# Optimization experiments

Hardware: AMD Instinct MI355X
Metric: run time of the kernel (lower is better)

The kernel has to match this reference:

```python
import jax, jax.numpy as jnp
import numpy as np

T, H = 2048, 1024          # tokens, hidden_size
NH, NKV, D = 16, 4, 64     # heads, kv heads, head_dim
E, F = 8, 1024             # experts, intermediate_size
TOPK = 1
EPS = 1e-5
THETA = 500000.0
SCALE = D ** -0.5


def rmsnorm(x, w=None, eps=EPS):
    # fp32 accumulation like vLLM RMSNorm
    v = jnp.mean(x.astype(jnp.float32) ** 2, axis=-1, keepdims=True)
    y = x.astype(jnp.float32) * jax.lax.rsqrt(v + eps)
    y = y.astype(x.dtype)
    return y * w if w is not None else y


def setup_inputs() -> dict:
    key = jax.random.key(0)
    ks = jax.random.split(key, 12)
    s = 1.0 / np.sqrt(H)
    sf = 1.0 / np.sqrt(F)
    return {
        "positions": jnp.arange(T, dtype=jnp.int32),
        "hidden_states": jax.random.normal(ks[0], (T, H), jnp.float32),
        "ln1_w": jnp.ones((H,), jnp.float32),
        "ln2_w": jnp.ones((H,), jnp.float32),
        "wqkv": jax.random.normal(ks[1], (H, (NH + 2 * NKV) * D), jnp.float32) * s,
        "wo": jax.random.normal(ks[2], (NH * D, H), jnp.float32) * s,
        "router_w": jax.random.normal(ks[3], (H, E), jnp.float32) * s,
        "w_gate": jax.random.normal(ks[4], (E, H, F), jnp.float32) * s,
        "w_up": jax.random.normal(ks[5], (E, H, F), jnp.float32) * s,
        "w_down": jax.random.normal(ks[6], (E, F, H), jnp.float32) * sf,
        "sh_gate": jax.random.normal(ks[7], (H, F), jnp.float32) * s,
        "sh_up": jax.random.normal(ks[8], (H, F), jnp.float32) * s,
        "sh_down": jax.random.normal(ks[9], (F, H), jnp.float32) * sf,
    }


def reference(positions, hidden_states, ln1_w, ln2_w, wqkv, wo, router_w,
              w_gate, w_up, w_down, sh_gate, sh_up, sh_down):
    # --- input_layernorm (residual is None on first call) ---
    residual = hidden_states
    h = rmsnorm(hidden_states, ln1_w)

    # --- attention: qkv proj ---
    qkv = h @ wqkv
    q = qkv[:, : NH * D].reshape(T, NH, D)
    k = qkv[:, NH * D: (NH + NKV) * D].reshape(T, NKV, D)
    v = qkv[:, (NH + NKV) * D:].reshape(T, NKV, D)

    # --- neox-style RoPE ---
    half = D // 2
    inv_freq = 1.0 / (THETA ** (jnp.arange(half, dtype=jnp.float32) / half))
    ang = positions.astype(jnp.float32)[:, None] * inv_freq[None, :]
    cos = jnp.cos(ang)[:, None, :]  # [T,1,half]
    sin = jnp.sin(ang)[:, None, :]

    def rope(x):
        x1, x2 = x[..., :half], x[..., half:]
        return jnp.concatenate([x1 * cos - x2 * sin, x2 * cos + x1 * sin], axis=-1)

    q = rope(q)
    k = rope(k)

    # --- fp32 QK-RMSNorm (no weight), applied after RoPE as in source ---
    q = rmsnorm(q)
    k = rmsnorm(k)

    # --- GQA causal attention ---
    n_rep = NH // NKV
    kr = jnp.repeat(k, n_rep, axis=1)  # [T,NH,D]
    vr = jnp.repeat(v, n_rep, axis=1)
    scores = jnp.einsum('thd,shd->hts', q, kr) * SCALE  # [NH,T,T]
    causal = positions[:, None] >= positions[None, :]
    scores = jnp.where(causal[None], scores, -jnp.inf)
    attn = jax.nn.softmax(scores, axis=-1)
    ao = jnp.einsum('hts,shd->thd', attn, vr).reshape(T, NH * D)
    h = ao @ wo

    # --- post_attention_layernorm with fused residual add ---
    x = h + residual
    residual = x
    h = rmsnorm(x, ln2_w)

    # --- MoE: top-1 sigmoid router, router weight applied on input ---
    logits = h @ router_w                      # [T,E]
    score, idx = jax.lax.top_k(logits, TOPK)   # [T,1]
    gate = jax.nn.sigmoid(score.astype(jnp.float32)).astype(h.dtype)
    x_in = h * gate                            # apply_router_weight_on_input
    onehot = (idx == jnp.arange(E)[None, :]).astype(h.dtype)  # [T,E]
    g = jax.nn.silu(jnp.einsum('th,ehf->tef', x_in, w_gate)) \
        * jnp.einsum('th,ehf->tef', x_in, w_up)               # [T,E,F]
    out_e = jnp.einsum('tef,efh->teh', g, w_down)             # [T,E,H]
    routed = jnp.einsum('teh,te->th', out_e, onehot)

    # --- shared expert (SiLU MLP) ---
    shared = (jax.nn.silu(h @ sh_gate) * (h @ sh_up)) @ sh_down

    out = routed + shared
    return (out, residual)
```

## Files before the change

kernel.cpp:

```cpp
#include <hip/hip_runtime.h>
#include <hip/hip_bf16.h>
#include <cmath>
#include <cstdint>

#define T 2048
#define H 1024
#define NH 16
#define NKV 4
#define DH 64
#define NE 8
#define FF 1024
#define QKVN ((NH + 2 * NKV) * DH)
#define EPS 1e-5f
#define ATTN_SCALE 0.125f
#define LOG2E 1.44269504f
#define MBOUND 12.0f
#define ASPLIT 4

typedef short bf16x8 __attribute__((ext_vector_type(8)));
typedef float floatx4 __attribute__((ext_vector_type(4)));

#define VMCNT(n) asm volatile("s_waitcnt vmcnt(" #n ")" ::: "memory")

__device__ __forceinline__ void gload16(const void* g, void* l) {
  __builtin_amdgcn_global_load_lds((const __attribute__((address_space(1))) void*)g,
                                   (__attribute__((address_space(3))) void*)l, 16, 0, 0);
}

__global__ __launch_bounds__(256) void rmsnorm1024(const float* __restrict__ x,
                                                   const float* __restrict__ w,
                                                   __hip_bfloat16* __restrict__ yb) {
  int row = blockIdx.x;
  const float4* x4 = (const float4*)(x + (size_t)row * H);
  float4 v = x4[threadIdx.x];
  float s = v.x * v.x + v.y * v.y + v.z * v.z + v.w * v.w;
  #pragma unroll
  for (int o = 32; o; o >>= 1) s += __shfl_down(s, o, 64);
  __shared__ float red[4];
  if ((threadIdx.x & 63) == 0) red[threadIdx.x >> 6] = s;
  __syncthreads();
  s = red[0] + red[1] + red[2] + red[3];
  float inv = rsqrtf(s * (1.0f / (float)H) + EPS);
  float4 wv = ((const float4*)w)[threadIdx.x];
  __hip_bfloat16* yp = yb + (size_t)row * H + threadIdx.x * 4;
  yp[0] = __float2bfloat16(v.x * inv * wv.x);
  yp[1] = __float2bfloat16(v.y * inv * wv.y);
  yp[2] = __float2bfloat16(v.z * inv * wv.z);
  yp[3] = __float2bfloat16(v.w * inv * wv.w);
}

__global__ __launch_bounds__(256) void fused_add_rms(const float* __restrict__ a,
                                                     const float* __restrict__ b,
                                                     float* __restrict__ resid,
                                                     const float* __restrict__ w,
                                                     float* __restrict__ yf,
                                                     __hip_bfloat16* __restrict__ yb,
                                                     int* __restrict__ counts_g) {
  int row = blockIdx.x;
  if (row == 0 && threadIdx.x < 2 * NE) counts_g[threadIdx.x] = 0;
  float4 av = ((const float4*)(a + (size_t)row * H))[threadIdx.x];
  float4 bv = ((const float4*)(b + (size_t)row * H))[threadIdx.x];
  float4 v = make_float4(av.x + bv.x, av.y + bv.y, av.z + bv.z, av.w + bv.w);
  ((float4*)(resid + (size_t)row * H))[threadIdx.x] = v;
  float s = v.x * v.x + v.y * v.y + v.z * v.z + v.w * v.w;
  #pragma unroll
  for (int o = 32; o; o >>= 1) s += __shfl_down(s, o, 64);
  __shared__ float red[4];
  if ((threadIdx.x & 63) == 0) red[threadIdx.x >> 6] = s;
  __syncthreads();
  s = red[0] + red[1] + red[2] + red[3];
  float inv = rsqrtf(s * (1.0f / (float)H) + EPS);
  float4 wv = ((const float4*)w)[threadIdx.x];
  float o0 = v.x * inv * wv.x, o1 = v.y * inv * wv.y, o2 = v.z * inv * wv.z, o3 = v.w * inv * wv.w;
  ((float4*)(yf + (size_t)row * H))[threadIdx.x] = make_float4(o0, o1, o2, o3);
  __hip_bfloat16* yp = yb + (size_t)row * H + threadIdx.x * 4;
  yp[0] = __float2bfloat16(o0);
  yp[1] = __float2bfloat16(o1);
  yp[2] = __float2bfloat16(o2);
  yp[3] = __float2bfloat16(o3);
}

__global__ __launch_bounds__(256) void tcast9(const float* __restrict__ srcE,
                                              const float* __restrict__ srcS,
                                              __hip_bfloat16* __restrict__ dst, int R, int C,
                                              long long srcStride, long long dstStride,
                                              long long sBatch, long long dBatch) {
  int z = blockIdx.z;
  const float* src = (srcS && z == (int)gridDim.z - 1) ? srcS : srcE + (long long)z * sBatch;
  dst += (long long)z * dBatch;
  int c0 = blockIdx.x * 64, r0 = blockIdx.y * 32;
  __shared__ float tile[32][65];
  int tid = threadIdx.x;
  int lr = tid >> 4;
  int lc = (tid & 15) * 4;
  #pragma unroll
  for (int it = 0; it < 2; it++) {
    float4 v = *(const float4*)(src + (long long)(r0 + lr + it * 16) * srcStride + c0 + lc);
    tile[lr + it * 16][lc + 0] = v.x;
    tile[lr + it * 16][lc + 1] = v.y;
    tile[lr + it * 16][lc + 2] = v.z;
    tile[lr + it * 16][lc + 3] = v.w;
  }
  __syncthreads();
  int oc = tid >> 2;
  int rr = (tid & 3) * 8;
  short ov[8];
  #pragma unroll
  for (int i = 0; i < 8; i++) {
    __hip_bfloat16 b = __float2bfloat16(tile[rr + i][oc]);
    ov[i] = *(short*)&b;
  }
  *(bf16x8*)((short*)dst + (long long)(c0 + oc) * dstStride + r0 + rr) = *(bf16x8*)ov;
}

__global__ __launch_bounds__(256) void gemm_bf16(const __hip_bfloat16* __restrict__ A,
                                                 const __hip_bfloat16* __restrict__ A2,
                                                 const __hip_bfloat16* __restrict__ Bt,
                                                 void* __restrict__ Cout, void* __restrict__ Cout2,
                                                 int M, int N, int K, int out_bf16,
                                                 const int* __restrict__ row_offs,
                                                 long long strideB,
                                                 const int* __restrict__ permA,
                                                 const float* __restrict__ gatev) {
  int e = blockIdx.z;
  bool sh = (A2 != nullptr && e == (int)gridDim.z - 1);
  int rbeg = 0, rend = M;
  const __hip_bfloat16* Ap = A;
  void* Cp = Cout;
  const int* pA = permA;
  if (sh) {
    Ap = A2; Cp = Cout2; pA = nullptr;
  } else if (row_offs) {
    rbeg = row_offs[e]; rend = row_offs[e + 1];
  }
  long long m0 = rbeg + (long long)blockIdx.y * 128;
  if (m0 >= rend) return;
  long long n0 = (long long)blockIdx.x * 64;
  const __hip_bfloat16* Bp = Bt + (long long)e * strideB;

  __shared__ unsigned short As[3 * 128 * 64];
  __shared__ unsigned short Bs[3 * 64 * 64];

  int tid = threadIdx.x;
  int lane = tid & 63, w = tid >> 6;
  int wr = (w >> 1) * 64, wc = (w & 1) * 32;
  int qd = lane >> 4, ln16 = lane & 15;
  int l7 = ln16 & 7;

  floatx4 acc[4][2];
  floatx4 zero = {0.f, 0.f, 0.f, 0.f};
  #pragma unroll
  for (int i = 0; i < 4; i++)
    #pragma unroll
    for (int j = 0; j < 2; j++) acc[i][j] = zero;

  int rowA[4], kcA[4];
  const unsigned short* Arow[4];
  const unsigned short* Brow[2];
  #pragma unroll
  for (int it = 0; it < 4; it++) {
    int chunk = tid + it * 256;
    rowA[it] = chunk >> 3;
    kcA[it] = ((chunk & 7) ^ (rowA[it] & 7)) * 8;
    long long ra = m0 + rowA[it];
    if (ra >= rend) ra = rend - 1;
    long long tok = pA ? (long long)pA[ra] : ra;
    Arow[it] = (const unsigned short*)Ap + tok * K;
  }
  #pragma unroll
  for (int it = 0; it < 2; it++)
    Brow[it] = (const unsigned short*)Bp + (n0 + rowA[it]) * K;

  auto stage = [&](int j) {
    int slot = j % 3;
    int kk = j << 6;
    unsigned short* Ad = As + slot * 8192;
    unsigned short* Bd = Bs + slot * 4096;
    #pragma unroll
    for (int it = 0; it < 4; it++)
      gload16(Arow[it] + kk + kcA[it], Ad + (tid + it * 256) * 8);
    #pragma unroll
    for (int it = 0; it < 2; it++)
      gload16(Brow[it] + kk + kcA[it], Bd + (tid + it * 256) * 8);
  };

  int NT = K >> 6;
  stage(0);
  if (NT > 1) { stage(1); VMCNT(6); } else { VMCNT(0); }
  __builtin_amdgcn_s_barrier();
  __builtin_amdgcn_sched_barrier(0);

  for (int k = 0; k < NT; k++) {
    if (k + 2 < NT) stage(k + 2);
    __builtin_amdgcn_sched_barrier(0);
    const unsigned short* Ac = As + (k % 3) * 8192;
    const unsigned short* Bc = Bs + (k % 3) * 4096;
    #pragma unroll
    for (int s = 0; s < 2; s++) {
      bf16x8 af[4], bfr[2];
      #pragma unroll
      for (int i = 0; i < 4; i++) {
        int row = wr + i * 16 + ln16;
        af[i] = *(const bf16x8*)(Ac + row * 64 + (((s * 4 + qd) ^ l7) * 8));
      }
      #pragma unroll
      for (int j = 0; j < 2; j++) {
        int row = wc + j * 16 + ln16;
        bfr[j] = *(const bf16x8*)(Bc + row * 64 + (((s * 4 + qd) ^ l7) * 8));
      }
      #pragma unroll
      for (int i = 0; i < 4; i++)
        #pragma unroll
        for (int j = 0; j < 2; j++)
          acc[i][j] = __builtin_amdgcn_mfma_f32_16x16x32_bf16(af[i], bfr[j], acc[i][j], 0, 0, 0);
    }
    if (k + 1 < NT) {
      if (k + 2 < NT) { VMCNT(6); } else { VMCNT(0); }
      __builtin_amdgcn_s_barrier();
      __builtin_amdgcn_sched_barrier(0);
    }
  }

  #pragma unroll
  for (int i = 0; i < 4; i++) {
    #pragma unroll
    for (int r = 0; r < 4; r++) {
      long long gm = m0 + wr + i * 16 + qd * 4 + r;
      if (gm < rend) {
        float gsc = 1.0f;
        if (pA && gatev) gsc = gatev[pA[gm]];
        #pragma unroll
        for (int j = 0; j < 2; j++) {
          long long gn = n0 + wc + j * 16 + ln16;
          float v = acc[i][j][r] * gsc;
          if (out_bf16)
            ((__hip_bfloat16*)Cp)[gm * N + gn] = __float2bfloat16(v);
          else
            ((float*)Cp)[gm * N + gn] = v;
        }
      }
    }
  }
}

__global__ __launch_bounds__(256) void rope_pack(const float* __restrict__ qkv,
                                                 const int* __restrict__ positions,
                                                 __hip_bfloat16* __restrict__ Qb,
                                                 __hip_bfloat16* __restrict__ Kb) {
  int b = blockIdx.x * 4 + (threadIdx.x >> 6);
  int t = b / (NH + NKV);
  int hh = b % (NH + NKV);
  const float* ptr = qkv + (long long)t * QKVN + hh * DH;
  int d = threadIdx.x & 63;
  float v = ptr[d];
  int fi = d & 31;
  float inv_freq = exp2f(-(float)fi * (18.93156857f / 32.0f));
  float ang = (float)positions[t] * inv_freq;
  float c = __cosf(ang), s = __sinf(ang);
  float other = __shfl_xor(v, 32, 64);
  float r = (d < 32) ? (v * c - other * s) : (v * c + other * s);
  float sq = r * r;
  #pragma unroll
  for (int off = 32; off; off >>= 1) sq += __shfl_xor(sq, off, 64);
  float o = r * rsqrtf(sq * (1.0f / (float)DH) + EPS);
  if (hh < NH)
    Qb[(size_t)t * (NH * DH) + hh * DH + d] = __float2bfloat16(o * (ATTN_SCALE * LOG2E));
  else
    Kb[(size_t)t * (NKV * DH) + (hh - NH) * DH + d] = __float2bfloat16(o);
}

__global__ __launch_bounds__(256, 2) void attn_mfma(const __hip_bfloat16* __restrict__ Qb,
                                                    const __hip_bfloat16* __restrict__ Kbuf,
                                                    const __hip_bfloat16* __restrict__ VtG,
                                                    float* __restrict__ Opart,
                                                    float* __restrict__ Lpart) {
  int kvh = blockIdx.y;
  int qi = blockIdx.x;
  int sp = blockIdx.z;
  int q0 = qi * 64;
  int nt = qi + 1;
  if (sp >= nt) return;
  int NT = (nt - 1 - sp) / ASPLIT + 1;

  __shared__ unsigned short Ks[3 * 64 * 64];
  __shared__ unsigned short Vs[3 * 64 * 64];
  __shared__ unsigned short Ps[4 * 16 * 64];

  int tid = threadIdx.x;
  int lane = tid & 63, w = tid >> 6;
  int h = kvh * 4 + w;
  int qd = lane >> 4, ln16 = lane & 15;
  int l7 = ln16 & 7;
  unsigned short* Pw = Ps + w * 16 * 64;

  int r0 = tid >> 3;
  int sc = ((tid & 7) ^ (r0 & 7)) * 8;

  const unsigned short* KbP = (const unsigned short*)Kbuf;
  const unsigned short* VtP = (const unsigned short*)VtG;

  auto stage = [&](int k) {
    int kb = (sp + k * ASPLIT) * 64;
    int slot = k % 3;
    unsigned short* Kd = Ks + slot * 4096;
    unsigned short* Vd = Vs + slot * 4096;
    gload16(KbP + (size_t)(kb + r0) * (NKV * DH) + kvh * DH + sc, Kd + tid * 8);
    gload16(KbP + (size_t)(kb + r0 + 32) * (NKV * DH) + kvh * DH + sc, Kd + tid * 8 + 2048);
    gload16(VtP + (size_t)(kvh * DH + r0) * T + kb + sc, Vd + tid * 8);
    gload16(VtP + (size_t)(kvh * DH + r0 + 32) * T + kb + sc, Vd + tid * 8 + 2048);
  };

  bf16x8 aq[4][2];
  #pragma unroll
  for (int rt = 0; rt < 4; rt++) {
    const unsigned short* qp =
        (const unsigned short*)Qb + (size_t)(q0 + rt * 16 + ln16) * (NH * DH) + h * DH;
    aq[rt][0] = *(const bf16x8*)(qp + qd * 8);
    aq[rt][1] = *(const bf16x8*)(qp + 32 + qd * 8);
  }

  bf16x8 ones;
  #pragma unroll
  for (int i = 0; i < 8; i++) ones[i] = (short)0x3F80;

  floatx4 O_[4][4], accl[4];
  floatx4 zero = {0.f, 0.f, 0.f, 0.f};
  #pragma unroll
  for (int rt = 0; rt < 4; rt++) {
    #pragma unroll
    for (int j = 0; j < 4; j++) O_[rt][j] = zero;
    accl[rt] = zero;
  }

  stage(0);
  if (NT > 1) { stage(1); VMCNT(4); } else { VMCNT(0); }
  __builtin_amdgcn_s_barrier();
  __builtin_amdgcn_sched_barrier(0);

  for (int k = 0; k < NT; k++) {
    if (k + 2 < NT) stage(k + 2);
    __builtin_amdgcn_sched_barrier(0);
    const unsigned short* Kc = Ks + (k % 3) * 4096;
    const unsigned short* Vc = Vs + (k % 3) * 4096;
    int kb = (sp + k * ASPLIT) * 64;

    #pragma unroll
    for (int rt = 0; rt < 4; rt++) {
      floatx4 S_[4];
      #pragma unroll
      for (int j = 0; j < 4; j++) S_[j] = zero;
      #pragma unroll
      for (int s = 0; s < 2; s++) {
        bf16x8 bk[4];
        #pragma unroll
        for (int j = 0; j < 4; j++)
          bk[j] = *(const bf16x8*)(Kc + (j * 16 + ln16) * 64 + (((s * 4 + qd) ^ l7) * 8));
        #pragma unroll
        for (int j = 0; j < 4; j++)
          S_[j] = __builtin_amdgcn_mfma_f32_16x16x32_bf16(aq[rt][s], bk[j], S_[j], 0, 0, 0);
      }

      int tq_base = q0 + rt * 16 + qd * 4;
      if (kb + 63 > q0 + rt * 16) {
        #pragma unroll
        for (int j = 0; j < 4; j++) {
          int tk = kb + j * 16 + ln16;
          #pragma unroll
          for (int r = 0; r < 4; r++)
            S_[j][r] = (tk <= tq_base + r) ? exp2f(S_[j][r] - MBOUND) : 0.f;
        }
      } else {
        #pragma unroll
        for (int j = 0; j < 4; j++)
          #pragma unroll
          for (int r = 0; r < 4; r++) S_[j][r] = exp2f(S_[j][r] - MBOUND);
      }

      #pragma unroll
      for (int j = 0; j < 4; j++)
        #pragma unroll
        for (int r = 0; r < 4; r++) {
          int row = qd * 4 + r;
          int pc = (((j * 2 + (ln16 >> 3)) ^ (row & 7)) * 8) + l7;
          __hip_bfloat16 pb = __float2bfloat16(S_[j][r]);
          Pw[row * 64 + pc] = *(unsigned short*)&pb;
        }

      #pragma unroll
      for (int s = 0; s < 2; s++) {
        bf16x8 ap = *(const bf16x8*)(Pw + ln16 * 64 + (((s * 4 + qd) ^ l7) * 8));
        bf16x8 bv[4];
        #pragma unroll
        for (int j = 0; j < 4; j++)
          bv[j] = *(const bf16x8*)(Vc + (j * 16 + ln16) * 64 + (((s * 4 + qd) ^ l7) * 8));
        #pragma unroll
        for (int j = 0; j < 4; j++)
          O_[rt][j] = __builtin_amdgcn_mfma_f32_16x16x32_bf16(ap, bv[j], O_[rt][j], 0, 0, 0);
        accl[rt] = __builtin_amdgcn_mfma_f32_16x16x32_bf16(ap, ones, accl[rt], 0, 0, 0);
      }
    }
    if (k + 1 < NT) {
      if (k + 2 < NT) { VMCNT(4); } else { VMCNT(0); }
      __builtin_amdgcn_s_barrier();
      __builtin_amdgcn_sched_barrier(0);
    }
  }

  size_t pbase = ((size_t)(qi * NH + h) * ASPLIT + sp) * (64 * 64);
  #pragma unroll
  for (int rt = 0; rt < 4; rt++) {
    int rl_base = rt * 16 + qd * 4;
    #pragma unroll
    for (int j = 0; j < 4; j++)
      #pragma unroll
      for (int r = 0; r < 4; r++)
        Opart[pbase + (size_t)(rl_base + r) * 64 + j * 16 + ln16] = O_[rt][j][r];
  }
  if (ln16 == 0) {
    size_t lbase = ((size_t)(qi * NH + h) * ASPLIT + sp) * 64;
    #pragma unroll
    for (int rt = 0; rt < 4; rt++)
      #pragma unroll
      for (int r = 0; r < 4; r++) Lpart[lbase + rt * 16 + qd * 4 + r] = accl[rt][r];
  }
}

__global__ __launch_bounds__(256) void attn_combine(const float* __restrict__ Opart,
                                                    const float* __restrict__ Lpart,
                                                    __hip_bfloat16* __restrict__ ao) {
  int qi = blockIdx.x, h = blockIdx.y;
  int nv = (qi + 1 < ASPLIT) ? (qi + 1) : ASPLIT;
  int row = threadIdx.x >> 2;
  int c0 = (threadIdx.x & 3) * 16;
  size_t base = (size_t)(qi * NH + h) * ASPLIT * 4096;
  size_t lb = (size_t)(qi * NH + h) * ASPLIT * 64;
  float l = 0.f;
  float acc[16];
  #pragma unroll
  for (int i = 0; i < 16; i++) acc[i] = 0.f;
  for (int s = 0; s < nv; s++) {
    const float* Op = Opart + base + (size_t)s * 4096 + (size_t)row * 64 + c0;
    l += Lpart[lb + s * 64 + row];
    #pragma unroll
    for (int i = 0; i < 16; i += 4) {
      float4 v = *(const float4*)(Op + i);
      acc[i] += v.x; acc[i + 1] += v.y; acc[i + 2] += v.z; acc[i + 3] += v.w;
    }
  }
  float inv = 1.f / l;
  int t = qi * 64 + row;
  short ov[16];
  #pragma unroll
  for (int i = 0; i < 16; i++) {
    __hip_bfloat16 b = __float2bfloat16(acc[i] * inv);
    ov[i] = *(short*)&b;
  }
  short* dst = (short*)ao + (size_t)t * (NH * DH) + h * DH + c0;
  *(bf16x8*)dst = *(bf16x8*)&ov[0];
  *(bf16x8*)(dst + 8) = *(bf16x8*)&ov[8];
}

__global__ void silumul_both(const __hip_bfloat16* __restrict__ gA2,
                             const __hip_bfloat16* __restrict__ gS2,
                             __hip_bfloat16* __restrict__ gP,
                             __hip_bfloat16* __restrict__ gPs, int n4each) {
  int i = blockIdx.x * blockDim.x + threadIdx.x;
  const __hip_bfloat16* src = gA2;
  __hip_bfloat16* dst = gP;
  if (i >= n4each) {
    i -= n4each;
    src = gS2;
    dst = gPs;
  }
  int el = i * 4;
  int row = el >> 10;
  int c = el & (FF - 1);
  const __hip_bfloat16* g = src + (size_t)row * (2 * FF) + c;
  #pragma unroll
  for (int k = 0; k < 4; k++) {
    float av = __bfloat162float(g[k]);
    float bv = __bfloat162float(g[FF + k]);
    dst[el + k] = __float2bfloat16(av / (1.f + __expf(-av)) * bv);
  }
}

__global__ __launch_bounds__(64) void router_kernel(const float* __restrict__ h2,
                                                    const float* __restrict__ rw,
                                                    int* __restrict__ idx,
                                                    float* __restrict__ gate,
                                                    int* __restrict__ counts) {
  int t = blockIdx.x;
  int lane = threadIdx.x;
  float acc[NE] = {};
  for (int k = lane; k < H; k += 64) {
    float hv = h2[(long long)t * H + k];
    float4 r0 = *(const float4*)(rw + (long long)k * NE);
    float4 r1 = *(const float4*)(rw + (long long)k * NE + 4);
    acc[0] += hv * r0.x; acc[1] += hv * r0.y; acc[2] += hv * r0.z; acc[3] += hv * r0.w;
    acc[4] += hv * r1.x; acc[5] += hv * r1.y; acc[6] += hv * r1.z; acc[7] += hv * r1.w;
  }
  #pragma unroll
  for (int off = 32; off; off >>= 1)
    #pragma unroll
    for (int e2 = 0; e2 < NE; e2++) acc[e2] += __shfl_down(acc[e2], off, 64);
  if (lane == 0) {
    int best = 0;
    float bv = acc[0];
    #pragma unroll
    for (int e2 = 1; e2 < NE; e2++)
      if (acc[e2] > bv) { bv = acc[e2]; best = e2; }
    idx[t] = best;
    gate[t] = 1.f / (1.f + expf(-bv));
    atomicAdd(&counts[best], 1);
  }
}

__global__ __launch_bounds__(256) void assign_scan(const int* __restrict__ counts,
                                                   const int* __restrict__ idx,
                                                   int* __restrict__ offs,
                                                   int* __restrict__ cnt2,
                                                   int* __restrict__ perm,
                                                   int* __restrict__ pos) {
  __shared__ int offs_s[NE + 1];
  if (threadIdx.x == 0) {
    int s = 0;
    for (int e2 = 0; e2 < NE; e2++) { offs_s[e2] = s; offs[e2] = s; s += counts[e2]; }
    offs_s[NE] = s; offs[NE] = s;
  }
  __syncthreads();
  for (int t = threadIdx.x; t < T; t += 256) {
    int e2 = idx[t];
    int p = offs_s[e2] + atomicAdd(&cnt2[e2], 1);
    pos[t] = p;
    perm[p] = t;
  }
}

__global__ __launch_bounds__(256) void final_add_kernel(float* __restrict__ out,
                                                        const float* __restrict__ outp,
                                                        const int* __restrict__ pos) {
  int t = blockIdx.x;
  int p = pos[t];
  const float4* src = (const float4*)(outp + (long long)p * H);
  float4* dst = (float4*)(out + (long long)t * H);
  float4 a = dst[threadIdx.x];
  float4 b = src[threadIdx.x];
  a.x += b.x; a.y += b.y; a.z += b.z; a.w += b.w;
  dst[threadIdx.x] = a;
}

extern "C" void kernel_launch(void* const* d_in, const int* in_sizes, int n_in,
                              void* d_out, int out_size, void* d_ws, size_t ws_size,
                              hipStream_t stream) {
  const int* positions = (const int*)d_in[0];
  const float* hidden = (const float*)d_in[1];
  const float* ln1_w = (const float*)d_in[2];
  const float* ln2_w = (const float*)d_in[3];
  const float* wqkv = (const float*)d_in[4];
  const float* wo = (const float*)d_in[5];
  const float* router_w = (const float*)d_in[6];
  const float* w_gate = (const float*)d_in[7];
  const float* w_up = (const float*)d_in[8];
  const float* w_down = (const float*)d_in[9];
  const float* sh_gate = (const float*)d_in[10];
  const float* sh_up = (const float*)d_in[11];
  const float* sh_down = (const float*)d_in[12];

  float* out = (float*)d_out;
  float* resid = out + (size_t)T * H;

  char* p = (char*)d_ws;
  auto alloc = [&](size_t bytes) { char* r = p; p += (bytes + 255) & ~(size_t)255; return r; };

  float* qkv = (float*)alloc((size_t)T * QKVN * 4);
  float* h2 = (float*)alloc((size_t)T * H * 4);
  float* gb1 = (float*)alloc((size_t)T * H * 4);
  float* outp = (float*)alloc((size_t)T * H * 4);
  __hip_bfloat16* h1b = (__hip_bfloat16*)alloc((size_t)T * H * 2);
  __hip_bfloat16* aob = (__hip_bfloat16*)alloc((size_t)T * H * 2);
  __hip_bfloat16* h2b = (__hip_bfloat16*)alloc((size_t)T * H * 2);
  __hip_bfloat16* gA2 = (__hip_bfloat16*)alloc((size_t)T * 2 * FF * 2);
  __hip_bfloat16* gP = (__hip_bfloat16*)alloc((size_t)T * FF * 2);
  __hip_bfloat16* Qb = (__hip_bfloat16*)alloc((size_t)T * NH * DH * 2);
  __hip_bfloat16* Kb = (__hip_bfloat16*)alloc((size_t)T * NKV * DH * 2);
  __hip_bfloat16* VtG = (__hip_bfloat16*)alloc((size_t)NKV * DH * T * 2);
  __hip_bfloat16* wqkvT = (__hip_bfloat16*)alloc((size_t)H * QKVN * 2);
  __hip_bfloat16* woT = (__hip_bfloat16*)alloc((size_t)H * H * 2);
  __hip_bfloat16* wguT = (__hip_bfloat16*)alloc((size_t)9 * 2 * FF * H * 2);
  __hip_bfloat16* wdT = (__hip_bfloat16*)alloc((size_t)9 * H * FF * 2);
  int* counts = (int*)alloc(2 * NE * 4);
  int* cnt2 = counts + NE;
  int* offs = (int*)alloc((NE + 1) * 4);
  int* idx = (int*)alloc(T * 4);
  int* perm = (int*)alloc(T * 4);
  int* pos = (int*)alloc(T * 4);
  float* gate = (float*)alloc(T * 4);

  __hip_bfloat16* gS2 = (__hip_bfloat16*)gb1;
  __hip_bfloat16* gPs = h1b;

  float* Opart = qkv;
  float* Lpart = qkv + (size_t)(T / 64) * NH * ASPLIT * 4096;

  tcast9<<<dim3(QKVN / 64, H / 32, 1), 256, 0, stream>>>(wqkv, nullptr, wqkvT, H, QKVN, QKVN, H, 0, 0);
  tcast9<<<dim3(H / 64, H / 32, 1), 256, 0, stream>>>(wo, nullptr, woT, H, H, H, H, 0, 0);
  tcast9<<<dim3(FF / 64, H / 32, 9), 256, 0, stream>>>(w_gate, sh_gate, wguT, H, FF, FF, H,
                                                       (long long)H * FF, (long long)2 * H * FF);
  tcast9<<<dim3(FF / 64, H / 32, 9), 256, 0, stream>>>(w_up, sh_up, wguT + (size_t)FF * H, H, FF, FF, H,
                                                       (long long)H * FF, (long long)2 * H * FF);
  tcast9<<<dim3(H / 64, FF / 32, 9), 256, 0, stream>>>(w_down, sh_down, wdT, FF, H, H, FF,
                                                       (long long)FF * H, (long long)H * FF);

  rmsnorm1024<<<T, 256, 0, stream>>>(hidden, ln1_w, h1b);
  gemm_bf16<<<dim3(QKVN / 64, T / 128, 1), 256, 0, stream>>>(h1b, nullptr, wqkvT, qkv, nullptr,
                                                             T, QKVN, H, 0, nullptr, 0, nullptr, nullptr);
  rope_pack<<<T * (NH + NKV) / 4, 256, 0, stream>>>(qkv, positions, Qb, Kb);
  tcast9<<<dim3(NKV * DH / 64, T / 32, 1), 256, 0, stream>>>(qkv + (NH + NKV) * DH, nullptr, VtG,
                                                             T, NKV * DH, QKVN, T, 0, 0);
  attn_mfma<<<dim3(T / 64, NKV, ASPLIT), 256, 0, stream>>>(Qb, Kb, VtG, Opart, Lpart);
  attn_combine<<<dim3(T / 64, NH), 256, 0, stream>>>(Opart, Lpart, aob);
  gemm_bf16<<<dim3(H / 64, T / 128, 1), 256, 0, stream>>>(aob, nullptr, woT, gb1, nullptr,
                                                          T, H, H, 0, nullptr, 0, nullptr, nullptr);
  fused_add_rms<<<T, 256, 0, stream>>>(gb1, hidden, resid, ln2_w, h2, h2b, counts);
  router_kernel<<<T, 64, 0, stream>>>(h2, router_w, idx, gate, counts);
  assign_scan<<<1, 256, 0, stream>>>(counts, idx, offs, cnt2, perm, pos);
  gemm_bf16<<<dim3(2 * FF / 64, T / 128, 9), 256, 0, stream>>>(h2b, h2b, wguT, gA2, gS2,
                                                               T, 2 * FF, H, 1, offs,
                                                               (long long)2 * H * FF, perm, gate);
  silumul_both<<<(2 * T * FF / 4) / 256, 256, 0, stream>>>(gA2, gS2, gP, gPs, T * FF / 4);
  gemm_bf16<<<dim3(H / 64, T / 128, 9), 256, 0, stream>>>(gP, gPs, wdT, outp, out,
                                                          T, H, FF, 0, offs, (long long)FF * H,
                                                          nullptr, nullptr);
  final_add_kernel<<<T, 256, 0, stream>>>(out, outp, pos);
}
```

Before: 432.3 us.

## Switch GEMM and attention to double-buffered LDS pipeline; vectorize silu-mul

```diff
diff --git a/kernel.cpp b/kernel.cpp
--- a/kernel.cpp
+++ b/kernel.cpp
@@ -19,8 +19,6 @@
 
 typedef short bf16x8 __attribute__((ext_vector_type(8)));
 typedef float floatx4 __attribute__((ext_vector_type(4)));
-
-#define VMCNT(n) asm volatile("s_waitcnt vmcnt(" #n ")" ::: "memory")
 
 __device__ __forceinline__ void gload16(const void* g, void* l) {
   __builtin_amdgcn_global_load_lds((const __attribute__((address_space(1))) void*)g,
@@ -138,8 +136,8 @@
   long long n0 = (long long)blockIdx.x * 64;
   const __hip_bfloat16* Bp = Bt + (long long)e * strideB;
 
-  __shared__ unsigned short As[3 * 128 * 64];
-  __shared__ unsigned short Bs[3 * 64 * 64];
+  __shared__ unsigned short As[2][128 * 64];
+  __shared__ unsigned short Bs[2][64 * 64];
 
   int tid = threadIdx.x;
   int lane = tid & 63, w = tid >> 6;
@@ -171,30 +169,27 @@
   for (int it = 0; it < 2; it++)
     Brow[it] = (const unsigned short*)Bp + (n0 + rowA[it]) * K;
 
-  auto stage = [&](int j) {
-    int slot = j % 3;
-    int kk = j << 6;
-    unsigned short* Ad = As + slot * 8192;
-    unsigned short* Bd = Bs + slot * 4096;
-    #pragma unroll
-    for (int it = 0; it < 4; it++)
-      gload16(Arow[it] + kk + kcA[it], Ad + (tid + it * 256) * 8);
-    #pragma unroll
-    for (int it = 0; it < 2; it++)
-      gload16(Brow[it] + kk + kcA[it], Bd + (tid + it * 256) * 8);
-  };
-
-  int NT = K >> 6;
-  stage(0);
-  if (NT > 1) { stage(1); VMCNT(6); } else { VMCNT(0); }
-  __builtin_amdgcn_s_barrier();
-  __builtin_amdgcn_sched_barrier(0);
-
-  for (int k = 0; k < NT; k++) {
-    if (k + 2 < NT) stage(k + 2);
-    __builtin_amdgcn_sched_barrier(0);
-    const unsigned short* Ac = As + (k % 3) * 8192;
-    const unsigned short* Bc = Bs + (k % 3) * 4096;
+  #pragma unroll
+  for (int it = 0; it < 4; it++)
+    gload16(Arow[it] + kcA[it], As[0] + (tid + it * 256) * 8);
+  #pragma unroll
+  for (int it = 0; it < 2; it++)
+    gload16(Brow[it] + kcA[it], Bs[0] + (tid + it * 256) * 8);
+  __syncthreads();
+
+  int cur = 0;
+  for (int k0 = 0; k0 < K; k0 += 64) {
+    int kn = k0 + 64;
+    if (kn < K) {
+      #pragma unroll
+      for (int it = 0; it < 4; it++)
+        gload16(Arow[it] + kn + kcA[it], As[cur ^ 1] + (tid + it * 256) * 8);
+      #pragma unroll
+      for (int it = 0; it < 2; it++)
+        gload16(Brow[it] + kn + kcA[it], Bs[cur ^ 1] + (tid + it * 256) * 8);
+    }
+    const unsigned short* Ac = As[cur];
+    const unsigned short* Bc = Bs[cur];
     #pragma unroll
     for (int s = 0; s < 2; s++) {
       bf16x8 af[4], bfr[2];
@@ -214,11 +209,8 @@
         for (int j = 0; j < 2; j++)
           acc[i][j] = __builtin_amdgcn_mfma_f32_16x16x32_bf16(af[i], bfr[j], acc[i][j], 0, 0, 0);
     }
-    if (k + 1 < NT) {
-      if (k + 2 < NT) { VMCNT(6); } else { VMCNT(0); }
-      __builtin_amdgcn_s_barrier();
-      __builtin_amdgcn_sched_barrier(0);
-    }
+    __syncthreads();
+    cur ^= 1;
   }
 
   #pragma unroll
@@ -280,10 +272,9 @@
   int q0 = qi * 64;
   int nt = qi + 1;
   if (sp >= nt) return;
-  int NT = (nt - 1 - sp) / ASPLIT + 1;
-
-  __shared__ unsigned short Ks[3 * 64 * 64];
-  __shared__ unsigned short Vs[3 * 64 * 64];
+
+  __shared__ unsigned short Ks[2][64 * 64];
+  __shared__ unsigned short Vs[2][64 * 64];
   __shared__ unsigned short Ps[4 * 16 * 64];
 
   int tid = threadIdx.x;
@@ -299,17 +290,6 @@
   const unsigned short* KbP = (const unsigned short*)Kbuf;
   const unsigned short* VtP = (const unsigned short*)VtG;
 
-  auto stage = [&](int k) {
-    int kb = (sp + k * ASPLIT) * 64;
-    int slot = k % 3;
-    unsigned short* Kd = Ks + slot * 4096;
-    unsigned short* Vd = Vs + slot * 4096;
-    gload16(KbP + (size_t)(kb + r0) * (NKV * DH) + kvh * DH + sc, Kd + tid * 8);
-    gload16(KbP + (size_t)(kb + r0 + 32) * (NKV * DH) + kvh * DH + sc, Kd + tid * 8 + 2048);
-    gload16(VtP + (size_t)(kvh * DH + r0) * T + kb + sc, Vd + tid * 8);
-    gload16(VtP + (size_t)(kvh * DH + r0 + 32) * T + kb + sc, Vd + tid * 8 + 2048);
-  };
-
   bf16x8 aq[4][2];
   #pragma unroll
   for (int rt = 0; rt < 4; rt++) {
@@ -332,17 +312,30 @@
     accl[rt] = zero;
   }
 
-  stage(0);
-  if (NT > 1) { stage(1); VMCNT(4); } else { VMCNT(0); }
-  __builtin_amdgcn_s_barrier();
-  __builtin_amdgcn_sched_barrier(0);
-
-  for (int k = 0; k < NT; k++) {
-    if (k + 2 < NT) stage(k + 2);
-    __builtin_amdgcn_sched_barrier(0);
-    const unsigned short* Kc = Ks + (k % 3) * 4096;
-    const unsigned short* Vc = Vs + (k % 3) * 4096;
-    int kb = (sp + k * ASPLIT) * 64;
+  {
+    int kb = sp * 64;
+    gload16(KbP + (size_t)(kb + r0) * (NKV * DH) + kvh * DH + sc, Ks[0] + tid * 8);
+    gload16(KbP + (size_t)(kb + r0 + 32) * (NKV * DH) + kvh * DH + sc, Ks[0] + tid * 8 + 2048);
+    gload16(VtP + (size_t)(kvh * DH + r0) * T + kb + sc, Vs[0] + tid * 8);
+    gload16(VtP + (size_t)(kvh * DH + r0 + 32) * T + kb + sc, Vs[0] + tid * 8 + 2048);
+  }
+  __syncthreads();
+
+  int cur = 0;
+  for (int kt = sp; kt < nt; kt += ASPLIT) {
+    int ktn = kt + ASPLIT;
+    if (ktn < nt) {
+      int kb = ktn * 64;
+      unsigned short* Kn = Ks[cur ^ 1];
+      unsigned short* Vn = Vs[cur ^ 1];
+      gload16(KbP + (size_t)(kb + r0) * (NKV * DH) + kvh * DH + sc, Kn + tid * 8);
+      gload16(KbP + (size_t)(kb + r0 + 32) * (NKV * DH) + kvh * DH + sc, Kn + tid * 8 + 2048);
+      gload16(VtP + (size_t)(kvh * DH + r0) * T + kb + sc, Vn + tid * 8);
+      gload16(VtP + (size_t)(kvh * DH + r0 + 32) * T + kb + sc, Vn + tid * 8 + 2048);
+    }
+    const unsigned short* Kc = Ks[cur];
+    const unsigned short* Vc = Vs[cur];
+    int kb = kt * 64;
 
     #pragma unroll
     for (int rt = 0; rt < 4; rt++) {
@@ -399,11 +392,8 @@
         accl[rt] = __builtin_amdgcn_mfma_f32_16x16x32_bf16(ap, ones, accl[rt], 0, 0, 0);
       }
     }
-    if (k + 1 < NT) {
-      if (k + 2 < NT) { VMCNT(4); } else { VMCNT(0); }
-      __builtin_amdgcn_s_barrier();
-      __builtin_amdgcn_sched_barrier(0);
-    }
+    __syncthreads();
+    cur ^= 1;
   }
 
   size_t pbase = ((size_t)(qi * NH + h) * ASPLIT + sp) * (64 * 64);
@@ -460,28 +450,35 @@
   *(bf16x8*)(dst + 8) = *(bf16x8*)&ov[8];
 }
 
-__global__ void silumul_both(const __hip_bfloat16* __restrict__ gA2,
-                             const __hip_bfloat16* __restrict__ gS2,
-                             __hip_bfloat16* __restrict__ gP,
-                             __hip_bfloat16* __restrict__ gPs, int n4each) {
+__global__ __launch_bounds__(256) void silumul_both(const __hip_bfloat16* __restrict__ gA2,
+                                                    const __hip_bfloat16* __restrict__ gS2,
+                                                    __hip_bfloat16* __restrict__ gP,
+                                                    __hip_bfloat16* __restrict__ gPs,
+                                                    int n8each) {
   int i = blockIdx.x * blockDim.x + threadIdx.x;
   const __hip_bfloat16* src = gA2;
   __hip_bfloat16* dst = gP;
-  if (i >= n4each) {
-    i -= n4each;
+  if (i >= n8each) {
+    i -= n8each;
     src = gS2;
     dst = gPs;
   }
-  int el = i * 4;
+  int el = i * 8;
   int row = el >> 10;
   int c = el & (FF - 1);
-  const __hip_bfloat16* g = src + (size_t)row * (2 * FF) + c;
-  #pragma unroll
-  for (int k = 0; k < 4; k++) {
-    float av = __bfloat162float(g[k]);
-    float bv = __bfloat162float(g[FF + k]);
-    dst[el + k] = __float2bfloat16(av / (1.f + __expf(-av)) * bv);
-  }
+  const unsigned short* g = (const unsigned short*)src + (size_t)row * (2 * FF) + c;
+  bf16x8 a8 = *(const bf16x8*)g;
+  bf16x8 b8 = *(const bf16x8*)(g + FF);
+  short o8[8];
+  #pragma unroll
+  for (int k = 0; k < 8; k++) {
+    short sa = a8[k], sb = b8[k];
+    float av = __bfloat162float(*(__hip_bfloat16*)&sa);
+    float bv = __bfloat162float(*(__hip_bfloat16*)&sb);
+    __hip_bfloat16 ob = __float2bfloat16(av / (1.f + __expf(-av)) * bv);
+    o8[k] = *(short*)&ob;
+  }
+  *(bf16x8*)((unsigned short*)dst + el) = *(bf16x8*)o8;
 }
 
 __global__ __launch_bounds__(64) void router_kernel(const float* __restrict__ h2,
@@ -627,7 +624,7 @@
   gemm_bf16<<<dim3(2 * FF / 64, T / 128, 9), 256, 0, stream>>>(h2b, h2b, wguT, gA2, gS2,
                                                                T, 2 * FF, H, 1, offs,
                                                                (long long)2 * H * FF, perm, gate);
-  silumul_both<<<(2 * T * FF / 4) / 256, 256, 0, stream>>>(gA2, gS2, gP, gPs, T * FF / 4);
+  silumul_both<<<(2 * T * FF / 8) / 256, 256, 0, stream>>>(gA2, gS2, gP, gPs, T * FF / 8);
   gemm_bf16<<<dim3(H / 64, T / 128, 9), 256, 0, stream>>>(gP, gPs, wdT, outp, out,
                                                           T, H, FF, 0, offs, (long long)FF * H,
                                                           nullptr, nullptr);
```

New measurement: 394.9 us. -8.6%, faster.
